# Optimization experiments

Hardware: AMD Instinct MI355X
Metric: run time of the kernel (lower is better)

## Reference

```python
import jax, jax.numpy as jnp
import numpy as np
from jax import lax

# Config matching init_kwargs
STRIDE = 1
PAD = 1


def setup_inputs() -> dict:
    key = jax.random.key(0)
    k1, k2, k3, k4 = jax.random.split(key, 4)
    x = jax.random.normal(k1, (8, 64, 128, 128), jnp.float32)
    # offset conv: out_channels = 2*kh*kw = 18, no bias; small init so offsets are moderate
    w_offset = jax.random.normal(k2, (18, 64, 3, 3), jnp.float32) * 0.01
    w_deform = jax.random.normal(k3, (64, 64, 3, 3), jnp.float32) * 0.05
    b_deform = jax.random.normal(k4, (64,), jnp.float32) * 0.05
    return {"x": x, "w_offset": w_offset, "w_deform": w_deform, "b_deform": b_deform}


def _deform_conv2d(x, offset, weight, bias, stride, pad):
    """torchvision.ops.deform_conv2d (v1, offset_groups=1) in pure jax.

    x: [B,C,H,W], offset: [B,2*kh*kw,Ho,Wo] ordered (dy,dx) per kernel tap,
    weight: [O,C,kh,kw], bias: [O].
    """
    B, C, H, W = x.shape
    O, _, kh, kw = weight.shape
    Ho, Wo = offset.shape[2], offset.shape[3]
    K = kh * kw

    off = offset.reshape(B, K, 2, Ho, Wo)  # [...,0]=dy, [...,1]=dx
    ky, kx = jnp.meshgrid(jnp.arange(kh), jnp.arange(kw), indexing="ij")
    base_y = (jnp.arange(Ho) * stride - pad).astype(x.dtype)  # [Ho]
    base_x = (jnp.arange(Wo) * stride - pad).astype(x.dtype)  # [Wo]
    # sampling positions [B,K,Ho,Wo]
    py = base_y[None, None, :, None] + ky.reshape(1, K, 1, 1).astype(x.dtype) + off[:, :, 0]
    px = base_x[None, None, None, :] + kx.reshape(1, K, 1, 1).astype(x.dtype) + off[:, :, 1]

    y0f = jnp.floor(py)
    x0f = jnp.floor(px)
    wy = py - y0f  # bilinear fractional weights [B,K,Ho,Wo]
    wx = px - x0f
    y0 = y0f.astype(jnp.int32)
    x0 = x0f.astype(jnp.int32)

    def gather(yi, xi):
        # zero-padded gather: out-of-bounds samples contribute 0
        valid = (yi >= 0) & (yi < H) & (xi >= 0) & (xi < W)
        yc = jnp.clip(yi, 0, H - 1)
        xc = jnp.clip(xi, 0, W - 1)
        # per-batch fancy gather -> [B, C, K, Ho, Wo]
        g = jax.vmap(lambda im, yy, xx: im[:, yy, xx])(x, yc, xc)
        return g * valid[:, None].astype(x.dtype)

    one = jnp.asarray(1, x.dtype)
    val = (gather(y0, x0) * ((one - wy) * (one - wx))[:, None]
           + gather(y0, x0 + 1) * ((one - wy) * wx)[:, None]
           + gather(y0 + 1, x0) * (wy * (one - wx))[:, None]
           + gather(y0 + 1, x0 + 1) * (wy * wx)[:, None])  # [B,C,K,Ho,Wo]

    out = jnp.einsum("ock,bckij->boij", weight.reshape(O, C, K), val)
    return out + bias[None, :, None, None]


def reference(x, w_offset, w_deform, b_deform):
    # offset-predicting conv (no bias)
    offset = lax.conv_general_dilated(
        x, w_offset, window_strides=(STRIDE, STRIDE),
        padding=[(PAD, PAD), (PAD, PAD)],
        dimension_numbers=("NCHW", "OIHW", "NCHW"))
    return _deform_conv2d(x, offset, w_deform, b_deform, STRIDE, PAD)
```

## Files before the change

### kernel.cpp

```cpp
#include <hip/hip_runtime.h>

#define BATCH 8
#define CIN 64
#define H 128
#define W 128
#define OCH 64
#define HW (H*W)
#define OFFCH 18

using f16x8 = __attribute__((ext_vector_type(8))) _Float16;
using f32x4 = __attribute__((ext_vector_type(4))) float;

static __device__ __forceinline__ int iclamp(int v, int lo, int hi) {
    return v < lo ? lo : (v > hi ? hi : v);
}
static __device__ __forceinline__ f16x8 splat8(_Float16 v) {
    return (f16x8){v, v, v, v, v, v, v, v};
}
static __device__ __forceinline__ unsigned packh2(float a, float b) {
    union { _Float16 h[2]; unsigned u; } pk;
    pk.h[0] = (_Float16)a; pk.h[1] = (_Float16)b;
    return pk.u;
}

__global__ __launch_bounds__(256) void transpose_x_kernel(
    const float* __restrict__ x, _Float16* __restrict__ xt)
{
    __shared__ float ls[CIN][129];
    int bid = blockIdx.x;
    int b = bid >> 7, y = bid & 127;
    int t = threadIdx.x;

    const float* xb = x + (size_t)b * CIN * HW + (size_t)y * W;
    #pragma unroll 4
    for (int i = 0; i < 32; ++i) {
        int c = i * 2 + (t >> 7);
        ls[c][t & 127] = xb[(size_t)c * HW + (t & 127)];
    }
    __syncthreads();

    _Float16* xo = xt + (size_t)(b * H + y) * W * CIN;
    #pragma unroll 4
    for (int i = 0; i < 16; ++i) {
        int px = i * 8 + (t >> 5);
        int c  = (t & 31) * 2;
        _Float16 a0 = (_Float16)ls[c][px];
        _Float16 a1 = (_Float16)ls[c + 1][px];
        union { _Float16 h[2]; unsigned int u; } pk;
        pk.h[0] = a0; pk.h[1] = a1;
        *(unsigned int*)&xo[(size_t)px * CIN + c] = pk.u;
    }
}

__global__ __launch_bounds__(256) void prep_wdf_kernel(
    const float* __restrict__ w, _Float16* __restrict__ wdf)
{
    int i = blockIdx.x * 256 + threadIdx.x;
    if (i >= 9 * 2 * 4 * 64 * 8) return;
    int j    = i & 7;
    int lane = (i >> 3) & 63;
    int mt   = (i >> 9) & 3;
    int cs   = (i >> 11) & 1;
    int tap  = i >> 12;
    int oc = mt * 16 + (lane & 15);
    int c  = cs * 32 + (lane >> 4) * 8 + j;
    wdf[i] = (_Float16)w[(oc * CIN + c) * 9 + tap];
}

__global__ __launch_bounds__(256) void prep_wof_kernel(
    const float* __restrict__ w, _Float16* __restrict__ wof)
{
    int i = blockIdx.x * 256 + threadIdx.x;
    if (i >= 9 * 2 * 2 * 64 * 8) return;
    int j    = i & 7;
    int lane = (i >> 3) & 63;
    int mt   = (i >> 9) & 1;
    int cs   = (i >> 10) & 1;
    int tap  = i >> 11;
    int oc = mt * 16 + (lane & 15);
    int c  = cs * 32 + (lane >> 4) * 8 + j;
    wof[i] = (oc < OFFCH) ? (_Float16)w[(oc * CIN + c) * 9 + tap] : (_Float16)0.f;
}

__global__ __launch_bounds__(1024, 4) void fused_deform_kernel(
    const _Float16* __restrict__ xt, const f16x8* __restrict__ wof,
    const f16x8* __restrict__ wdf, const float* __restrict__ bias,
    float* __restrict__ out)
{
    __shared__ _Float16 band[6 * 128 * CIN];
    __shared__ uint4 recs[16 * 16 * 9];
    __shared__ unsigned int offs_f[16 * 16 * 9];

    int bid  = blockIdx.x;
    int b    = bid & 7;
    int y    = (bid >> 3) * 2;
    int tid  = threadIdx.x;
    int lane = tid & 63;
    int wave = tid >> 6;
    int l15  = lane & 15;
    int lk   = lane >> 4;
    int yo   = y + (wave >> 3);
    int p    = (wave & 7) * 16 + l15;

    int ylo = y - 2 < 0 ? 0 : y - 2;
    int yhi = y + 3 > H - 1 ? H - 1 : y + 3;
    int nrm1 = yhi - ylo;

    const _Float16* xb = xt + (size_t)b * HW * CIN;

    {
        int spx = tid >> 3;
        int sjl = tid & 7;
        int sjp = sjl ^ (spx & 7);
        #pragma unroll
        for (int r = 0; r < 6; ++r) {
            int gy = ylo + r;
            if (gy > yhi) break;
            *(f16x8*)&band[(((size_t)r * 128 + spx) * 8 + sjp) * 8] =
                *(const f16x8*)&xb[((size_t)gy * W + spx) * CIN + sjl * 8];
        }
    }
    __syncthreads();

    f32x4 oacc[2];
    oacc[0] = (f32x4){0.f, 0.f, 0.f, 0.f};
    oacc[1] = (f32x4){0.f, 0.f, 0.f, 0.f};

    #pragma unroll
    for (int tap = 0; tap < 9; ++tap) {
        int ky = tap / 3, kx = tap - 3 * ky;
        int yy = yo - 1 + ky;
        int pos = p - 1 + kx;
        bool inb = (yy >= 0 && yy < H && pos >= 0 && pos < W);
        int ry = yy - ylo;
        #pragma unroll
        for (int cs = 0; cs < 2; ++cs) {
            const f16x8* wf = wof + (size_t)((tap * 2 + cs) * 2) * 64 + lane;
            f16x8 a0 = wf[0];
            f16x8 a1 = wf[64];
            f16x8 bfrag = splat8((_Float16)0.f);
            if (inb) {
                int jp = (cs * 4 + lk) ^ (pos & 7);
                bfrag = *(const f16x8*)&band[(((size_t)ry * 128 + pos) * 8 + jp) * 8];
            }
            oacc[0] = __builtin_amdgcn_mfma_f32_16x16x32_f16(a0, bfrag, oacc[0], 0, 0, 0);
            oacc[1] = __builtin_amdgcn_mfma_f32_16x16x32_f16(a1, bfrag, oacc[1], 0, 0, 0);
        }
    }

    int rbase = (wave * 16 + l15) * 9;
    auto build = [&](int tap, float offy, float offx) {
        int ky = tap / 3, kx = tap - 3 * ky;
        float py  = (float)(yo - 1 + ky) + offy;
        float pxf = (float)(p  - 1 + kx) + offx;
        float y0f = floorf(py), x0f = floorf(pxf);
        float fy = py - y0f, fx = pxf - x0f;
        int y0 = (int)y0f, x0 = (int)x0f;
        int y1 = y0 + 1, x1 = x0 + 1;
        float m00 = (1.f - fy) * (1.f - fx);
        float m01 = (1.f - fy) * fx;
        float m10 = fy * (1.f - fx);
        float m11 = fy * fx;
        if (y0 < 0 || y0 >= H) { m00 = 0.f; m01 = 0.f; }
        if (y1 < 0 || y1 >= H) { m10 = 0.f; m11 = 0.f; }
        if (x0 < 0 || x0 >= W) { m00 = 0.f; m10 = 0.f; }
        if (x1 < 0 || x1 >= W) { m01 = 0.f; m11 = 0.f; }
        int y0c = iclamp(y0, 0, H - 1), y1c = iclamp(y1, 0, H - 1);
        int x0c = iclamp(x0, 0, W - 1), x1c = iclamp(x1, 0, W - 1);
        int ry0 = y0c - ylo, ry1 = y1c - ylo;
        unsigned o0 = (ry0 < 0 || ry0 > nrm1) ? 0x8000u : 0u;
        unsigned o1 = (ry1 < 0 || ry1 > nrm1) ? 0x8000u : 0u;
        int r0 = iclamp(ry0, 0, 5), r1 = iclamp(ry1, 0, 5);
        unsigned f0 = (unsigned)(((r0 * 128 + x0c) << 3) | (x0c & 7)) | o0;
        unsigned f1 = (unsigned)(((r0 * 128 + x1c) << 3) | (x1c & 7)) | o0;
        unsigned f2 = (unsigned)(((r1 * 128 + x0c) << 3) | (x0c & 7)) | o1;
        unsigned f3 = (unsigned)(((r1 * 128 + x1c) << 3) | (x1c & 7)) | o1;
        uint4 rc;
        rc.x = packh2(m00, m01);
        rc.y = packh2(m10, m11);
        rc.z = f0 | (f1 << 16);
        rc.w = f2 | (f3 << 16);
        recs[rbase + tap] = rc;
        offs_f[rbase + tap] = packh2(offy, offx);
    };
    build(2 * lk,     oacc[0][0], oacc[0][1]);
    build(2 * lk + 1, oacc[0][2], oacc[0][3]);
    if (lk == 0) build(8, oacc[1][0], oacc[1][1]);

    f32x4 acc[4];
    #pragma unroll
    for (int mt = 0; mt < 4; ++mt) acc[mt] = (f32x4){0.f, 0.f, 0.f, 0.f};

    const char* bb = (const char*)band;

    #pragma unroll
    for (int tap = 0; tap < 9; ++tap) {
        uint4 rc = recs[rbase + tap];
        union { unsigned u; _Float16 h[2]; } mA, mB;
        mA.u = rc.x; mB.u = rc.y;
        _Float16 h00 = mA.h[0], h01 = mA.h[1], h10 = mB.h[0], h11 = mB.h[1];
        int f0 = rc.z & 0xffff, f1 = rc.z >> 16;
        int f2 = rc.w & 0xffff, f3 = rc.w >> 16;
        bool fall = ((rc.z | rc.w) & 0x8000u) != 0;
        int a00 = (((f0 >> 3) & 1023) << 7) + ((lk ^ (f0 & 7)) << 4);
        int a01 = (((f1 >> 3) & 1023) << 7) + ((lk ^ (f1 & 7)) << 4);
        int a10 = (((f2 >> 3) & 1023) << 7) + ((lk ^ (f2 & 7)) << 4);
        int a11 = (((f3 >> 3) & 1023) << 7) + ((lk ^ (f3 & 7)) << 4);

        f16x8 bf0, bf1;
        {
            f16x8 g00 = *(const f16x8*)(bb + a00);
            f16x8 g01 = *(const f16x8*)(bb + a01);
            f16x8 g10 = *(const f16x8*)(bb + a10);
            f16x8 g11 = *(const f16x8*)(bb + a11);
            bf0 = g00 * splat8(h00) + g01 * splat8(h01)
                + g10 * splat8(h10) + g11 * splat8(h11);
            f16x8 k00 = *(const f16x8*)(bb + (a00 ^ 64));
            f16x8 k01 = *(const f16x8*)(bb + (a01 ^ 64));
            f16x8 k10 = *(const f16x8*)(bb + (a10 ^ 64));
            f16x8 k11 = *(const f16x8*)(bb + (a11 ^ 64));
            bf1 = k00 * splat8(h00) + k01 * splat8(h01)
                + k10 * splat8(h10) + k11 * splat8(h11);
        }
        if (fall) {
            union { unsigned u; _Float16 h[2]; } of;
            of.u = offs_f[rbase + tap];
            float offy = (float)of.h[0], offx = (float)of.h[1];
            int ky = tap / 3, kx = tap - 3 * ky;
            float py  = (float)(yo - 1 + ky) + offy;
            float pxf = (float)(p  - 1 + kx) + offx;
            float y0f = floorf(py), x0f = floorf(pxf);
            float fy = py - y0f, fx = pxf - x0f;
            int y0 = (int)y0f, x0 = (int)x0f;
            int y1 = y0 + 1, x1 = x0 + 1;
            float n00 = (1.f - fy) * (1.f - fx);
            float n01 = (1.f - fy) * fx;
            float n10 = fy * (1.f - fx);
            float n11 = fy * fx;
            if (y0 < 0 || y0 >= H) { n00 = 0.f; n01 = 0.f; }
            if (y1 < 0 || y1 >= H) { n10 = 0.f; n11 = 0.f; }
            if (x0 < 0 || x0 >= W) { n00 = 0.f; n10 = 0.f; }
            if (x1 < 0 || x1 >= W) { n01 = 0.f; n11 = 0.f; }
            int y0c = iclamp(y0, 0, H - 1), y1c = iclamp(y1, 0, H - 1);
            int x0c = iclamp(x0, 0, W - 1), x1c = iclamp(x1, 0, W - 1);
            _Float16 q00 = (_Float16)n00, q01 = (_Float16)n01;
            _Float16 q10 = (_Float16)n10, q11 = (_Float16)n11;
            size_t i00 = ((size_t)y0c * W + x0c) * CIN, i01 = ((size_t)y0c * W + x1c) * CIN;
            size_t i10 = ((size_t)y1c * W + x0c) * CIN, i11 = ((size_t)y1c * W + x1c) * CIN;
            int c0 = lk * 8;
            bf0 = (*(const f16x8*)&xb[i00 + c0]) * splat8(q00)
                + (*(const f16x8*)&xb[i01 + c0]) * splat8(q01)
                + (*(const f16x8*)&xb[i10 + c0]) * splat8(q10)
                + (*(const f16x8*)&xb[i11 + c0]) * splat8(q11);
            int c1 = 32 + lk * 8;
            bf1 = (*(const f16x8*)&xb[i00 + c1]) * splat8(q00)
                + (*(const f16x8*)&xb[i01 + c1]) * splat8(q01)
                + (*(const f16x8*)&xb[i10 + c1]) * splat8(q10)
                + (*(const f16x8*)&xb[i11 + c1]) * splat8(q11);
        }

        #pragma unroll
        for (int cs = 0; cs < 2; ++cs) {
            f16x8 bfrag = cs ? bf1 : bf0;
            const f16x8* wf = wdf + (size_t)((tap * 2 + cs) * 4) * 64 + lane;
            #pragma unroll
            for (int mt = 0; mt < 4; ++mt)
                acc[mt] = __builtin_amdgcn_mfma_f32_16x16x32_f16(
                    wf[mt * 64], bfrag, acc[mt], 0, 0, 0);
        }
    }

    #pragma unroll
    for (int mt = 0; mt < 4; ++mt) {
        #pragma unroll
        for (int r = 0; r < 4; ++r) {
            int oc = mt * 16 + lk * 4 + r;
            out[((size_t)b * OCH + oc) * HW + (size_t)yo * W + p] = acc[mt][r] + bias[oc];
        }
    }
}

extern "C" void kernel_launch(void* const* d_in, const int* in_sizes, int n_in,
                              void* d_out, int out_size, void* d_ws, size_t ws_size,
                              hipStream_t stream) {
    const float* x     = (const float*)d_in[0];
    const float* w_off = (const float*)d_in[1];
    const float* w_def = (const float*)d_in[2];
    const float* b_def = (const float*)d_in[3];
    float* out = (float*)d_out;

    _Float16* xt  = (_Float16*)d_ws;
    _Float16* wdf = xt + (size_t)BATCH * HW * CIN;
    _Float16* wof = wdf + 36864;

    transpose_x_kernel<<<BATCH * H, 256, 0, stream>>>(x, xt);
    prep_wdf_kernel<<<(36864 + 255) / 256, 256, 0, stream>>>(w_def, wdf);
    prep_wof_kernel<<<(18432 + 255) / 256, 256, 0, stream>>>(w_off, wof);
    fused_deform_kernel<<<BATCH * H / 2, 1024, 0, stream>>>(
        xt, (const f16x8*)wof, (const f16x8*)wdf, b_def, out);
}
```

Baseline: 58.39 us.

## Halve block size and give each wave two pixel tiles to reuse weight fragments

Each wave now processes 32 pixels as two 16-wide N tiles instead of 16, so the block drops from 1024 to 512 threads while still covering two output rows. Each loaded weight A-fragment (offset conv and deform conv) feeds two MFMAs, halving weight-fragment global/cache loads per output. The band staging loop is split into two passes per row. This raises register pressure (doubled accumulators and B fragments) and reduces threads per block, which may lower latency hiding.

```diff
diff --git a/kernel.cpp b/kernel.cpp
--- a/kernel.cpp
+++ b/kernel.cpp
@@ -82,14 +82,14 @@
     wof[i] = (oc < OFFCH) ? (_Float16)w[(oc * CIN + c) * 9 + tap] : (_Float16)0.f;
 }
 
-__global__ __launch_bounds__(1024, 4) void fused_deform_kernel(
+__global__ __launch_bounds__(512, 2) void fused_deform_kernel(
     const _Float16* __restrict__ xt, const f16x8* __restrict__ wof,
     const f16x8* __restrict__ wdf, const float* __restrict__ bias,
     float* __restrict__ out)
 {
     __shared__ _Float16 band[6 * 128 * CIN];
-    __shared__ uint4 recs[16 * 16 * 9];
-    __shared__ unsigned int offs_f[16 * 16 * 9];
+    __shared__ uint4 recs[2 * 128 * 9];
+    __shared__ unsigned int offs_f[2 * 128 * 9];
 
     int bid  = blockIdx.x;
     int b    = bid & 7;
@@ -99,8 +99,11 @@
     int wave = tid >> 6;
     int l15  = lane & 15;
     int lk   = lane >> 4;
-    int yo   = y + (wave >> 3);
-    int p    = (wave & 7) * 16 + l15;
+    int rw   = wave >> 2;
+    int yo   = y + rw;
+    int pxbase = (wave & 3) * 32;
+    int p0   = pxbase + l15;
+    int p1   = p0 + 16;
 
     int ylo = y - 2 < 0 ? 0 : y - 2;
     int yhi = y + 3 > H - 1 ? H - 1 : y + 3;
@@ -109,47 +112,61 @@
     const _Float16* xb = xt + (size_t)b * HW * CIN;
 
     {
-        int spx = tid >> 3;
-        int sjl = tid & 7;
-        int sjp = sjl ^ (spx & 7);
         #pragma unroll
         for (int r = 0; r < 6; ++r) {
             int gy = ylo + r;
             if (gy > yhi) break;
-            *(f16x8*)&band[(((size_t)r * 128 + spx) * 8 + sjp) * 8] =
-                *(const f16x8*)&xb[((size_t)gy * W + spx) * CIN + sjl * 8];
+            #pragma unroll
+            for (int i = 0; i < 2; ++i) {
+                int linear = i * 512 + tid;
+                int spx = linear >> 3;
+                int sjl = linear & 7;
+                int sjp = sjl ^ (spx & 7);
+                *(f16x8*)&band[(((size_t)r * 128 + spx) * 8 + sjp) * 8] =
+                    *(const f16x8*)&xb[((size_t)gy * W + spx) * CIN + sjl * 8];
+            }
         }
     }
     __syncthreads();
 
-    f32x4 oacc[2];
-    oacc[0] = (f32x4){0.f, 0.f, 0.f, 0.f};
-    oacc[1] = (f32x4){0.f, 0.f, 0.f, 0.f};
+    f32x4 oacc[2][2];
+    #pragma unroll
+    for (int mt = 0; mt < 2; ++mt)
+        #pragma unroll
+        for (int nt = 0; nt < 2; ++nt) oacc[mt][nt] = (f32x4){0.f, 0.f, 0.f, 0.f};
 
     #pragma unroll
     for (int tap = 0; tap < 9; ++tap) {
         int ky = tap / 3, kx = tap - 3 * ky;
         int yy = yo - 1 + ky;
-        int pos = p - 1 + kx;
-        bool inb = (yy >= 0 && yy < H && pos >= 0 && pos < W);
+        bool iny = (yy >= 0 && yy < H);
         int ry = yy - ylo;
+        int pos0 = p0 - 1 + kx;
+        int pos1 = p1 - 1 + kx;
         #pragma unroll
         for (int cs = 0; cs < 2; ++cs) {
             const f16x8* wf = wof + (size_t)((tap * 2 + cs) * 2) * 64 + lane;
             f16x8 a0 = wf[0];
             f16x8 a1 = wf[64];
-            f16x8 bfrag = splat8((_Float16)0.f);
-            if (inb) {
-                int jp = (cs * 4 + lk) ^ (pos & 7);
-                bfrag = *(const f16x8*)&band[(((size_t)ry * 128 + pos) * 8 + jp) * 8];
-            }
-            oacc[0] = __builtin_amdgcn_mfma_f32_16x16x32_f16(a0, bfrag, oacc[0], 0, 0, 0);
-            oacc[1] = __builtin_amdgcn_mfma_f32_16x16x32_f16(a1, bfrag, oacc[1], 0, 0, 0);
-        }
-    }
-
-    int rbase = (wave * 16 + l15) * 9;
-    auto build = [&](int tap, float offy, float offx) {
+            f16x8 b0 = splat8((_Float16)0.f), b1 = splat8((_Float16)0.f);
+            if (iny && pos0 >= 0 && pos0 < W) {
+                int jp = (cs * 4 + lk) ^ (pos0 & 7);
+                b0 = *(const f16x8*)&band[(((size_t)ry * 128 + pos0) * 8 + jp) * 8];
+            }
+            if (iny && pos1 >= 0 && pos1 < W) {
+                int jp = (cs * 4 + lk) ^ (pos1 & 7);
+                b1 = *(const f16x8*)&band[(((size_t)ry * 128 + pos1) * 8 + jp) * 8];
+            }
+            oacc[0][0] = __builtin_amdgcn_mfma_f32_16x16x32_f16(a0, b0, oacc[0][0], 0, 0, 0);
+            oacc[1][0] = __builtin_amdgcn_mfma_f32_16x16x32_f16(a1, b0, oacc[1][0], 0, 0, 0);
+            oacc[0][1] = __builtin_amdgcn_mfma_f32_16x16x32_f16(a0, b1, oacc[0][1], 0, 0, 0);
+            oacc[1][1] = __builtin_amdgcn_mfma_f32_16x16x32_f16(a1, b1, oacc[1][1], 0, 0, 0);
+        }
+    }
+
+    int rbase0 = (rw * 128 + p0) * 9;
+    int rbase1 = (rw * 128 + p1) * 9;
+    auto build = [&](int tap, float offy, float offx, int p, int rbase) {
         int ky = tap / 3, kx = tap - 3 * ky;
         float py  = (float)(yo - 1 + ky) + offy;
         float pxf = (float)(p  - 1 + kx) + offx;
@@ -183,99 +200,115 @@
         recs[rbase + tap] = rc;
         offs_f[rbase + tap] = packh2(offy, offx);
     };
-    build(2 * lk,     oacc[0][0], oacc[0][1]);
-    build(2 * lk + 1, oacc[0][2], oacc[0][3]);
-    if (lk == 0) build(8, oacc[1][0], oacc[1][1]);
-
-    f32x4 acc[4];
-    #pragma unroll
-    for (int mt = 0; mt < 4; ++mt) acc[mt] = (f32x4){0.f, 0.f, 0.f, 0.f};
+    build(2 * lk,     oacc[0][0][0], oacc[0][0][1], p0, rbase0);
+    build(2 * lk + 1, oacc[0][0][2], oacc[0][0][3], p0, rbase0);
+    build(2 * lk,     oacc[0][1][0], oacc[0][1][1], p1, rbase1);
+    build(2 * lk + 1, oacc[0][1][2], oacc[0][1][3], p1, rbase1);
+    if (lk == 0) {
+        build(8, oacc[1][0][0], oacc[1][0][1], p0, rbase0);
+        build(8, oacc[1][1][0], oacc[1][1][1], p1, rbase1);
+    }
+
+    f32x4 acc[4][2];
+    #pragma unroll
+    for (int mt = 0; mt < 4; ++mt)
+        #pragma unroll
+        for (int nt = 0; nt < 2; ++nt) acc[mt][nt] = (f32x4){0.f, 0.f, 0.f, 0.f};
 
     const char* bb = (const char*)band;
 
     #pragma unroll
     for (int tap = 0; tap < 9; ++tap) {
-        uint4 rc = recs[rbase + tap];
-        union { unsigned u; _Float16 h[2]; } mA, mB;
-        mA.u = rc.x; mB.u = rc.y;
-        _Float16 h00 = mA.h[0], h01 = mA.h[1], h10 = mB.h[0], h11 = mB.h[1];
-        int f0 = rc.z & 0xffff, f1 = rc.z >> 16;
-        int f2 = rc.w & 0xffff, f3 = rc.w >> 16;
-        bool fall = ((rc.z | rc.w) & 0x8000u) != 0;
-        int a00 = (((f0 >> 3) & 1023) << 7) + ((lk ^ (f0 & 7)) << 4);
-        int a01 = (((f1 >> 3) & 1023) << 7) + ((lk ^ (f1 & 7)) << 4);
-        int a10 = (((f2 >> 3) & 1023) << 7) + ((lk ^ (f2 & 7)) << 4);
-        int a11 = (((f3 >> 3) & 1023) << 7) + ((lk ^ (f3 & 7)) << 4);
-
-        f16x8 bf0, bf1;
-        {
+        f16x8 bfr[2][2];
+        #pragma unroll
+        for (int nt = 0; nt < 2; ++nt) {
+            int rbase = nt ? rbase1 : rbase0;
+            int pp    = nt ? p1 : p0;
+            uint4 rc = recs[rbase + tap];
+            union { unsigned u; _Float16 h[2]; } mA, mB;
+            mA.u = rc.x; mB.u = rc.y;
+            _Float16 h00 = mA.h[0], h01 = mA.h[1], h10 = mB.h[0], h11 = mB.h[1];
+            int f0 = rc.z & 0xffff, f1 = rc.z >> 16;
+            int f2 = rc.w & 0xffff, f3 = rc.w >> 16;
+            bool fall = ((rc.z | rc.w) & 0x8000u) != 0;
+            int a00 = (((f0 >> 3) & 1023) << 7) + ((lk ^ (f0 & 7)) << 4);
+            int a01 = (((f1 >> 3) & 1023) << 7) + ((lk ^ (f1 & 7)) << 4);
+            int a10 = (((f2 >> 3) & 1023) << 7) + ((lk ^ (f2 & 7)) << 4);
+            int a11 = (((f3 >> 3) & 1023) << 7) + ((lk ^ (f3 & 7)) << 4);
+
             f16x8 g00 = *(const f16x8*)(bb + a00);
             f16x8 g01 = *(const f16x8*)(bb + a01);
             f16x8 g10 = *(const f16x8*)(bb + a10);
             f16x8 g11 = *(const f16x8*)(bb + a11);
-            bf0 = g00 * splat8(h00) + g01 * splat8(h01)
-                + g10 * splat8(h10) + g11 * splat8(h11);
+            bfr[0][nt] = g00 * splat8(h00) + g01 * splat8(h01)
+                       + g10 * splat8(h10) + g11 * splat8(h11);
             f16x8 k00 = *(const f16x8*)(bb + (a00 ^ 64));
             f16x8 k01 = *(const f16x8*)(bb + (a01 ^ 64));
             f16x8 k10 = *(const f16x8*)(bb + (a10 ^ 64));
             f16x8 k11 = *(const f16x8*)(bb + (a11 ^ 64));
-            bf1 = k00 * splat8(h00) + k01 * splat8(h01)
-                + k10 * splat8(h10) + k11 * splat8(h11);
-        }
-        if (fall) {
-            union { unsigned u; _Float16 h[2]; } of;
-            of.u = offs_f[rbase + tap];
-            float offy = (float)of.h[0], offx = (float)of.h[1];
-            int ky = tap / 3, kx = tap - 3 * ky;
-            float py  = (float)(yo - 1 + ky) + offy;
-            float pxf = (float)(p  - 1 + kx) + offx;
-            float y0f = floorf(py), x0f = floorf(pxf);
-            float fy = py - y0f, fx = pxf - x0f;
-            int y0 = (int)y0f, x0 = (int)x0f;
-            int y1 = y0 + 1, x1 = x0 + 1;
-            float n00 = (1.f - fy) * (1.f - fx);
-            float n01 = (1.f - fy) * fx;
-            float n10 = fy * (1.f - fx);
-            float n11 = fy * fx;
-            if (y0 < 0 || y0 >= H) { n00 = 0.f; n01 = 0.f; }
-            if (y1 < 0 || y1 >= H) { n10 = 0.f; n11 = 0.f; }
-            if (x0 < 0 || x0 >= W) { n00 = 0.f; n10 = 0.f; }
-            if (x1 < 0 || x1 >= W) { n01 = 0.f; n11 = 0.f; }
-            int y0c = iclamp(y0, 0, H - 1), y1c = iclamp(y1, 0, H - 1);
-            int x0c = iclamp(x0, 0, W - 1), x1c = iclamp(x1, 0, W - 1);
-            _Float16 q00 = (_Float16)n00, q01 = (_Float16)n01;
-            _Float16 q10 = (_Float16)n10, q11 = (_Float16)n11;
-            size_t i00 = ((size_t)y0c * W + x0c) * CIN, i01 = ((size_t)y0c * W + x1c) * CIN;
-            size_t i10 = ((size_t)y1c * W + x0c) * CIN, i11 = ((size_t)y1c * W + x1c) * CIN;
-            int c0 = lk * 8;
-            bf0 = (*(const f16x8*)&xb[i00 + c0]) * splat8(q00)
-                + (*(const f16x8*)&xb[i01 + c0]) * splat8(q01)
-                + (*(const f16x8*)&xb[i10 + c0]) * splat8(q10)
-                + (*(const f16x8*)&xb[i11 + c0]) * splat8(q11);
-            int c1 = 32 + lk * 8;
-            bf1 = (*(const f16x8*)&xb[i00 + c1]) * splat8(q00)
-                + (*(const f16x8*)&xb[i01 + c1]) * splat8(q01)
-                + (*(const f16x8*)&xb[i10 + c1]) * splat8(q10)
-                + (*(const f16x8*)&xb[i11 + c1]) * splat8(q11);
+            bfr[1][nt] = k00 * splat8(h00) + k01 * splat8(h01)
+                       + k10 * splat8(h10) + k11 * splat8(h11);
+
+            if (fall) {
+                union { unsigned u; _Float16 h[2]; } of;
+                of.u = offs_f[rbase + tap];
+                float offy = (float)of.h[0], offx = (float)of.h[1];
+                int ky = tap / 3, kx = tap - 3 * ky;
+                float py  = (float)(yo - 1 + ky) + offy;
+                float pxf = (float)(pp - 1 + kx) + offx;
+                float y0f = floorf(py), x0f = floorf(pxf);
+                float fy = py - y0f, fx = pxf - x0f;
+                int y0 = (int)y0f, x0 = (int)x0f;
+                int y1 = y0 + 1, x1 = x0 + 1;
+                float n00 = (1.f - fy) * (1.f - fx);
+                float n01 = (1.f - fy) * fx;
+                float n10 = fy * (1.f - fx);
+                float n11 = fy * fx;
+                if (y0 < 0 || y0 >= H) { n00 = 0.f; n01 = 0.f; }
+                if (y1 < 0 || y1 >= H) { n10 = 0.f; n11 = 0.f; }
+                if (x0 < 0 || x0 >= W) { n00 = 0.f; n10 = 0.f; }
+                if (x1 < 0 || x1 >= W) { n01 = 0.f; n11 = 0.f; }
+                int y0c = iclamp(y0, 0, H - 1), y1c = iclamp(y1, 0, H - 1);
+                int x0c = iclamp(x0, 0, W - 1), x1c = iclamp(x1, 0, W - 1);
+                _Float16 q00 = (_Float16)n00, q01 = (_Float16)n01;
+                _Float16 q10 = (_Float16)n10, q11 = (_Float16)n11;
+                size_t i00 = ((size_t)y0c * W + x0c) * CIN, i01 = ((size_t)y0c * W + x1c) * CIN;
+                size_t i10 = ((size_t)y1c * W + x0c) * CIN, i11 = ((size_t)y1c * W + x1c) * CIN;
+                int c0 = lk * 8;
+                bfr[0][nt] = (*(const f16x8*)&xb[i00 + c0]) * splat8(q00)
+                           + (*(const f16x8*)&xb[i01 + c0]) * splat8(q01)
+                           + (*(const f16x8*)&xb[i10 + c0]) * splat8(q10)
+                           + (*(const f16x8*)&xb[i11 + c0]) * splat8(q11);
+                int c1 = 32 + lk * 8;
+                bfr[1][nt] = (*(const f16x8*)&xb[i00 + c1]) * splat8(q00)
+                           + (*(const f16x8*)&xb[i01 + c1]) * splat8(q01)
+                           + (*(const f16x8*)&xb[i10 + c1]) * splat8(q10)
+                           + (*(const f16x8*)&xb[i11 + c1]) * splat8(q11);
+            }
         }
 
         #pragma unroll
         for (int cs = 0; cs < 2; ++cs) {
-            f16x8 bfrag = cs ? bf1 : bf0;
             const f16x8* wf = wdf + (size_t)((tap * 2 + cs) * 4) * 64 + lane;
             #pragma unroll
-            for (int mt = 0; mt < 4; ++mt)
-                acc[mt] = __builtin_amdgcn_mfma_f32_16x16x32_f16(
-                    wf[mt * 64], bfrag, acc[mt], 0, 0, 0);
+            for (int mt = 0; mt < 4; ++mt) {
+                f16x8 af = wf[mt * 64];
+                acc[mt][0] = __builtin_amdgcn_mfma_f32_16x16x32_f16(af, bfr[cs][0], acc[mt][0], 0, 0, 0);
+                acc[mt][1] = __builtin_amdgcn_mfma_f32_16x16x32_f16(af, bfr[cs][1], acc[mt][1], 0, 0, 0);
+            }
         }
     }
 
     #pragma unroll
     for (int mt = 0; mt < 4; ++mt) {
         #pragma unroll
-        for (int r = 0; r < 4; ++r) {
-            int oc = mt * 16 + lk * 4 + r;
-            out[((size_t)b * OCH + oc) * HW + (size_t)yo * W + p] = acc[mt][r] + bias[oc];
+        for (int nt = 0; nt < 2; ++nt) {
+            int pp = nt ? p1 : p0;
+            #pragma unroll
+            for (int r = 0; r < 4; ++r) {
+                int oc = mt * 16 + lk * 4 + r;
+                out[((size_t)b * OCH + oc) * HW + (size_t)yo * W + pp] = acc[mt][nt][r] + bias[oc];
+            }
         }
     }
 }
@@ -296,6 +329,6 @@
     transpose_x_kernel<<<BATCH * H, 256, 0, stream>>>(x, xt);
     prep_wdf_kernel<<<(36864 + 255) / 256, 256, 0, stream>>>(w_def, wdf);
     prep_wof_kernel<<<(18432 + 255) / 256, 256, 0, stream>>>(w_off, wof);
-    fused_deform_kernel<<<BATCH * H / 2, 1024, 0, stream>>>(
+    fused_deform_kernel<<<BATCH * H / 2, 512, 0, stream>>>(
         xt, (const f16x8*)wof, (const f16x8*)wdf, b_def, out);
 }
```

Result: faster. 55.12 us (-5.6%).
